# Kernel optimization log

Hardware: AMD Instinct MI355X
Metric: run time of the kernel (lower is better)

The kernel has to match this reference:

```python
import jax, jax.numpy as jnp
import numpy as np

K = 2  # DGL TAGConv default number of hops
N_GRAPHS = 64


def _tag_conv(h, src, dst, W, b, norm):
    # TAGConv: concat [h, A_hat h, A_hat^2 h] @ W + b, A_hat = D^-1/2 A D^-1/2
    n = h.shape[0]
    hops = [h]
    cur = h
    for _ in range(K):
        msg = (cur * norm)[src]                      # gather from src, [E, d]
        agg = jnp.zeros_like(cur).at[dst].add(msg)   # scatter-sum to dst
        cur = agg * norm
        hops.append(cur)
    z = jnp.concatenate(hops, axis=-1)               # [N, (K+1)*d]
    return jax.nn.relu(z @ W + b)


def _norm(dst, n):
    deg = jnp.zeros((n,), jnp.float32).at[dst].add(1.0)
    deg = jnp.clip(deg, 1.0, None)
    return (deg ** -0.5)[:, None]                    # [N, 1]


def setup_inputs() -> dict:
    key = jax.random.key(0)
    ks = jax.random.split(key, 8)
    N, E, IN, HID, C = 100000, 3200000, 128, 256, 10
    h = jax.random.normal(ks[0], (N, IN), jnp.float32)
    src = jax.random.randint(ks[1], (E,), 0, N, jnp.int32)
    dst = jax.random.randint(ks[2], (E,), 0, N, jnp.int32)
    graph_ids = jnp.sort(jax.random.randint(ks[3], (N,), 0, N_GRAPHS, jnp.int32))
    s1 = ((K + 1) * IN) ** -0.5
    s2 = ((K + 1) * HID) ** -0.5
    W1 = jax.random.normal(ks[4], ((K + 1) * IN, HID), jnp.float32) * s1
    b1 = jnp.zeros((HID,), jnp.float32)
    W2 = jax.random.normal(ks[5], ((K + 1) * HID, HID), jnp.float32) * s2
    b2 = jnp.zeros((HID,), jnp.float32)
    Wc = jax.random.normal(ks[6], (HID, C), jnp.float32) * (HID ** -0.5)
    bc = jnp.zeros((C,), jnp.float32)
    return {"h": h, "src": src, "dst": dst, "graph_ids": graph_ids,
            "W1": W1, "b1": b1, "W2": W2, "b2": b2, "Wc": Wc, "bc": bc}


def reference(h, src, dst, graph_ids, W1, b1, W2, b2, Wc, bc):
    n = h.shape[0]
    norm = _norm(dst, n)
    x = _tag_conv(h, src, dst, W1, b1, norm)
    x = _tag_conv(x, src, dst, W2, b2, norm)
    pooled = jax.ops.segment_max(x, graph_ids, num_segments=N_GRAPHS)  # [G, HID]
    return pooled @ Wc + bc                                            # [G, C]
```

## Files before the change

### kernel.cpp

```cpp
#include <hip/hip_runtime.h>
#include <hip/hip_bf16.h>


typedef unsigned short u16;
typedef unsigned int u32;
typedef unsigned char u8;

__device__ inline float u2f(u16 u) { return __uint_as_float(((u32)u) << 16); }
__device__ inline u16 f2u(float f) {
    __hip_bfloat16 b = __float2bfloat16(f);
    return *reinterpret_cast<u16*>(&b);
}


constexpr int NPB = 128, NC = 128, NBMAX = 784;

__global__ __launch_bounds__(256) void countA_kernel(
    const int* __restrict__ dst, int* __restrict__ Hmat, int E, int CS, int NB) {
    __shared__ int hist[NBMAX];
    int tid = threadIdx.x;
    for (int b = tid; b < NB; b += 256) hist[b] = 0;
    __syncthreads();
    int base = blockIdx.x * CS;
    int end = base + CS < E ? base + CS : E;
    for (int i = base + tid; i < end; i += 256) {
        int d = __builtin_nontemporal_load(dst + i);
        atomicAdd(&hist[d >> 7], 1);
    }
    __syncthreads();
    for (int b = tid; b < NB; b += 256) Hmat[b * NC + blockIdx.x] = hist[b];
}

__global__ __launch_bounds__(256) void scatterC_kernel(
    const int* __restrict__ src, const int* __restrict__ dst,
    const int* __restrict__ Omat, uint2* __restrict__ Earr,
    int E, int CS, int NB) {
    __shared__ int cur[NBMAX];
    int tid = threadIdx.x;
    int c = blockIdx.x;
    for (int b = tid; b < NB; b += 256) cur[b] = Omat[b * NC + c];
    __syncthreads();
    int base = c * CS;
    int end = base + CS < E ? base + CS : E;
    for (int i = base + tid; i < end; i += 256) {
        int d = __builtin_nontemporal_load(dst + i);
        int s = __builtin_nontemporal_load(src + i);
        int pos = atomicAdd(&cur[d >> 7], 1);
        uint2 e;
        e.x = (u32)s;
        e.y = (u32)(d & (NPB - 1));
        Earr[pos] = e;
    }
}

__global__ __launch_bounds__(256) void fineD_kernel(
    const uint2* __restrict__ Earr, const int* __restrict__ Omat,
    int* __restrict__ colidx, int* __restrict__ rowptr,
    float* __restrict__ normv, int N, int E, int NB) {
    __shared__ int cnt[NPB];
    __shared__ int scn[NPB];
    __shared__ int cur2[NPB];
    int tid = threadIdx.x;
    int b = blockIdx.x;
    int base = Omat[b * NC];
    int end = Omat[(b + 1) * NC];
    if (tid < NPB) cnt[tid] = 0;
    __syncthreads();
    for (int i = base + tid; i < end; i += 256)
        atomicAdd(&cnt[Earr[i].y], 1);
    __syncthreads();
    if (tid < NPB) scn[tid] = cnt[tid];
    __syncthreads();
    for (int off = 1; off < NPB; off <<= 1) {
        int v = (tid < NPB && tid >= off) ? scn[tid - off] : 0;
        __syncthreads();
        if (tid < NPB) scn[tid] += v;
        __syncthreads();
    }
    int node0 = b * NPB;
    if (tid < NPB) {
        int excl = scn[tid] - cnt[tid];
        cur2[tid] = base + excl;
        int node = node0 + tid;
        if (node < N) {
            rowptr[node] = base + excl;
            int d = cnt[tid];
            float fd = d < 1 ? 1.0f : (float)d;
            normv[node] = rsqrtf(fd);
        }
    }
    if (b == 0 && tid == 0) rowptr[N] = E;
    __syncthreads();
    for (int i = base + tid; i < end; i += 256) {
        uint2 e = Earr[i];
        int pos = atomicAdd(&cur2[e.y], 1);
        colidx[pos] = (int)e.x;
    }
}

__global__ void scan1_kernel(const int* __restrict__ in, int* __restrict__ outp,
                             int* __restrict__ bsum, int n) {
    __shared__ int sd[1024];
    int t = threadIdx.x;
    int i = blockIdx.x * 1024 + t;
    int v = (i < n) ? in[i] : 0;
    sd[t] = v;
    __syncthreads();
    for (int off = 1; off < 1024; off <<= 1) {
        int x = (t >= off) ? sd[t - off] : 0;
        __syncthreads();
        sd[t] += x;
        __syncthreads();
    }
    if (i < n) outp[i] = sd[t] - v;
    if (t == 1023) bsum[blockIdx.x] = sd[t];
}

__global__ void scan2_kernel(int* __restrict__ bsum, int nb) {
    __shared__ int sd[1024];
    int t = threadIdx.x;
    int v = (t < nb) ? bsum[t] : 0;
    sd[t] = v;
    __syncthreads();
    for (int off = 1; off < 1024; off <<= 1) {
        int x = (t >= off) ? sd[t - off] : 0;
        __syncthreads();
        sd[t] += x;
        __syncthreads();
    }
    if (t < nb) bsum[t] = sd[t] - v;
}

__global__ void scan3_kernel(int* __restrict__ outp, const int* __restrict__ bsum,
                             int n, int E) {
    int i = blockIdx.x * blockDim.x + threadIdx.x;
    if (i < n) outp[i] += bsum[i >> 10];
    if (i == 0) outp[n] = E;
}


struct alignas(4) U2 { u16 v[2]; };
struct alignas(8) U4 { u16 v[4]; };
struct alignas(16) U8 { u16 v[8]; };


__global__ __launch_bounds__(256) void castquant_f32_128(
    const float* __restrict__ h, u16* __restrict__ cat, int ldcat,
    const float* __restrict__ normv,
    u8* __restrict__ q, float* __restrict__ m, int N) {
    int row = blockIdx.x * 4 + (threadIdx.x >> 6);
    if (row >= N) return;
    int lane = threadIdx.x & 63;
    float2 f = *(const float2*)(h + (size_t)row * 128 + lane * 2);
    U2 o;
    o.v[0] = f2u(f.x);
    o.v[1] = f2u(f.y);
    *(U2*)(cat + (size_t)row * ldcat + lane * 2) = o;
    float mx = fmaxf(fabsf(f.x), fabsf(f.y));
    #pragma unroll
    for (int off = 32; off > 0; off >>= 1)
        mx = fmaxf(mx, __shfl_xor(mx, off, 64));
    float inv = mx > 0.f ? 127.f / mx : 0.f;
    u32 q0 = (u32)((int)rintf(f.x * inv) + 128);
    u32 q1 = (u32)((int)rintf(f.y * inv) + 128);
    *(unsigned short*)(q + (size_t)row * 128 + lane * 2) =
        (unsigned short)(q0 | (q1 << 8));
    if (lane == 0) m[row] = normv[row] * (mx * (1.f / 127.f));
}


__global__ __launch_bounds__(256) void quant_bf16_256(
    const u16* __restrict__ x, const float* __restrict__ normv,
    u8* __restrict__ q, float* __restrict__ m, int N) {
    int row = blockIdx.x * 4 + (threadIdx.x >> 6);
    if (row >= N) return;
    int lane = threadIdx.x & 63;
    U4 v = *(const U4*)(x + (size_t)row * 256 + lane * 4);
    float f[4];
    #pragma unroll
    for (int i = 0; i < 4; ++i) f[i] = u2f(v.v[i]);
    float mx = fmaxf(fmaxf(fabsf(f[0]), fabsf(f[1])),
                     fmaxf(fabsf(f[2]), fabsf(f[3])));
    #pragma unroll
    for (int off = 32; off > 0; off >>= 1)
        mx = fmaxf(mx, __shfl_xor(mx, off, 64));
    float inv = mx > 0.f ? 127.f / mx : 0.f;
    u32 b0 = (u32)((int)rintf(f[0] * inv) + 128);
    u32 b1 = (u32)((int)rintf(f[1] * inv) + 128);
    u32 b2 = (u32)((int)rintf(f[2] * inv) + 128);
    u32 b3 = (u32)((int)rintf(f[3] * inv) + 128);
    *(u32*)(q + (size_t)row * 256 + lane * 4) =
        b0 | (b1 << 8) | (b2 << 16) | (b3 << 24);
    if (lane == 0) m[row] = normv[row] * (mx * (1.f / 127.f));
}


template <int BPL, int QOUT>
__global__ __launch_bounds__(256, 2) void prop_q8_kernel(
    const u8* __restrict__ qin, const float* __restrict__ m,
    u16* __restrict__ out, int ldout,
    const int* __restrict__ rowptr, const int* __restrict__ colidx,
    const float* __restrict__ normv, int N,
    u8* __restrict__ qout, float* __restrict__ mout) {
    constexpr int D = 32 * BPL;
    constexpr int NW = BPL / 4;
    constexpr int UE = 8;
    int node = blockIdx.x * 4 + (threadIdx.x >> 6);
    if (node >= N) return;
    const int lane = threadIdx.x & 63;
    const int half = lane >> 5;
    const int l32 = lane & 31;
    const u32 laneoff = (u32)l32 * BPL;
    int s = rowptr[node], e = rowptr[node + 1];
    float acc[BPL];
    #pragma unroll
    for (int q = 0; q < BPL; ++q) acc[q] = 0.f;
    float msum = 0.f;
    const int nfull = (e - s) >> 4;
    int p = s;
    if (nfull > 0) {
        int c[UE];
        #pragma unroll
        for (int u = 0; u < UE; ++u) c[u] = colidx[s + 2 * u + half];
        for (int g = 0; g < nfull; ++g) {
            u32 w[UE][NW];
            #pragma unroll
            for (int u = 0; u < UE; ++u) {
                u32 off = (u32)c[u] * D + laneoff;
                if (BPL == 8) {
                    uint2 gg = *(const uint2*)(qin + off);
                    w[u][0] = gg.x; w[u][1] = gg.y;
                } else {
                    w[u][0] = *(const u32*)(qin + off);
                }
            }
            float nm[UE];
            #pragma unroll
            for (int u = 0; u < UE; ++u) nm[u] = m[c[u]];
            if (g + 1 < nfull) {
                int pn = s + (g + 1) * 16;
                #pragma unroll
                for (int u = 0; u < UE; ++u) c[u] = colidx[pn + 2 * u + half];
            }
            #pragma unroll
            for (int u = 0; u < UE; ++u) {
                msum += nm[u];
                #pragma unroll
                for (int t = 0; t < NW; ++t) {
                    u32 ww = w[u][t];
                    acc[4 * t + 0] += nm[u] * (float)(ww & 0xffu);
                    acc[4 * t + 1] += nm[u] * (float)((ww >> 8) & 0xffu);
                    acc[4 * t + 2] += nm[u] * (float)((ww >> 16) & 0xffu);
                    acc[4 * t + 3] += nm[u] * (float)(ww >> 24);
                }
            }
        }
        p = s + nfull * 16;
    }
    if (p < e) {
        const int el = e - 1;
        int c[UE];
        #pragma unroll
        for (int u = 0; u < UE; ++u) {
            int idx = p + 2 * u + half;
            c[u] = colidx[idx < e ? idx : el];
        }
        u32 w[UE][NW];
        #pragma unroll
        for (int u = 0; u < UE; ++u) {
            u32 off = (u32)c[u] * D + laneoff;
            if (BPL == 8) {
                uint2 gg = *(const uint2*)(qin + off);
                w[u][0] = gg.x; w[u][1] = gg.y;
            } else {
                w[u][0] = *(const u32*)(qin + off);
            }
        }
        float nm[UE];
        #pragma unroll
        for (int u = 0; u < UE; ++u) {
            int idx = p + 2 * u + half;
            float mm = m[c[u]];
            nm[u] = idx < e ? mm : 0.f;
        }
        #pragma unroll
        for (int u = 0; u < UE; ++u) {
            msum += nm[u];
            #pragma unroll
            for (int t = 0; t < NW; ++t) {
                u32 ww = w[u][t];
                acc[4 * t + 0] += nm[u] * (float)(ww & 0xffu);
                acc[4 * t + 1] += nm[u] * (float)((ww >> 8) & 0xffu);
                acc[4 * t + 2] += nm[u] * (float)((ww >> 16) & 0xffu);
                acc[4 * t + 3] += nm[u] * (float)(ww >> 24);
            }
        }
    }
    #pragma unroll
    for (int q = 0; q < BPL; ++q) acc[q] += __shfl_xor(acc[q], 32, 64);
    msum += __shfl_xor(msum, 32, 64);
    float nn = normv[node];
    #pragma unroll
    for (int q = 0; q < BPL; ++q) acc[q] = nn * (acc[q] - 128.f * msum);
    if (half == 0) {
        if (BPL == 8) {
            U8 o;
            #pragma unroll
            for (int q = 0; q < 8; ++q) o.v[q] = f2u(acc[q]);
            *(U8*)(out + (size_t)node * ldout + l32 * 8) = o;
        } else {
            U4 o;
            #pragma unroll
            for (int q = 0; q < 4; ++q) o.v[q] = f2u(acc[q]);
            *(U4*)(out + (size_t)node * ldout + l32 * 4) = o;
        }
    }
    if (QOUT) {
        float mx = 0.f;
        #pragma unroll
        for (int q = 0; q < BPL; ++q) mx = fmaxf(mx, fabsf(acc[q]));
        #pragma unroll
        for (int off = 16; off > 0; off >>= 1)
            mx = fmaxf(mx, __shfl_xor(mx, off, 64));
        float inv = mx > 0.f ? 127.f / mx : 0.f;
        if (half == 0) {
            u32 b[BPL > 4 ? 8 : 4];
            #pragma unroll
            for (int q = 0; q < BPL; ++q)
                b[q] = (u32)((int)rintf(acc[q] * inv) + 128);
            if (BPL == 8) {
                uint2 g;
                g.x = b[0] | (b[1] << 8) | (b[2] << 16) | (b[3] << 24);
                g.y = b[4] | (b[5] << 8) | (b[6] << 16) | (b[7] << 24);
                *(uint2*)(qout + (size_t)node * D + l32 * 8) = g;
            } else {
                *(u32*)(qout + (size_t)node * D + l32 * 4) =
                    b[0] | (b[1] << 8) | (b[2] << 16) | (b[3] << 24);
            }
            if (lane == 0) mout[node] = nn * (mx * (1.f / 127.f));
        }
    }
}


typedef __attribute__((ext_vector_type(8))) short bf16x8f;
typedef __attribute__((ext_vector_type(4))) float f32x4;

__device__ inline void async16(const void* g, void* l) {
    __builtin_amdgcn_global_load_lds(
        (__attribute__((address_space(1))) void*)(g),
        (__attribute__((address_space(3))) void*)(l), 16, 0, 0);
}

constexpr int GBM = 128, GBN = 128, GBK = 32, KH = 128;

template <int KK>
__global__ __launch_bounds__(256, 2) void gemm_mfma(
    const u16* __restrict__ A, int lda,
    const u16* __restrict__ Bt,
    const u16* __restrict__ Cadd,
    const float* __restrict__ bias,
    u16* __restrict__ Cout,
    int M, int relu) {
    constexpr int NPH = KK / KH;
    __shared__ u16 Ab[GBM * KH];
    __shared__ u16 Bb[GBN * KH];
    const int tid = threadIdx.x;
    const int lane = tid & 63;
    const int wave = tid >> 6;
    const int wm = wave >> 1, wn = wave & 1;
    int nwg = gridDim.x;
    int qq = nwg >> 3, rr = nwg & 7;
    int xcd = blockIdx.x & 7, wi = blockIdx.x >> 3;
    int nb = (xcd < rr ? xcd * (qq + 1) : rr * (qq + 1) + (xcd - rr) * qq) + wi;
    const int row0 = (nb >> 1) * GBM;
    const int col0 = (nb & 1) * GBN;
    const int NOUT = 256;

    f32x4 acc[4][4];
    #pragma unroll
    for (int mi = 0; mi < 4; ++mi)
        #pragma unroll
        for (int ni = 0; ni < 4; ++ni) acc[mi][ni] = (f32x4)0.f;

    const int mb = lane & 15;
    const int seg4 = lane >> 4;

    for (int ph = 0; ph < NPH; ++ph) {
        if (ph) __syncthreads();
        #pragma unroll
        for (int i = 0; i < 8; ++i) {
            int c = tid + i * 256;
            int row = c >> 4;
            int sg = (c & 15) ^ (row & 7);
            async16(A + (size_t)(row0 + row) * lda + ph * KH + sg * 8,
                    Ab + c * 8);
        }
        #pragma unroll
        for (int i = 0; i < 8; ++i) {
            int c = tid + i * 256;
            int row = c >> 4;
            int sg = (c & 15) ^ (row & 7);
            async16(Bt + (size_t)(col0 + row) * KK + ph * KH + sg * 8,
                    Bb + c * 8);
        }
        __syncthreads();
        #pragma unroll
        for (int ks = 0; ks < KH / GBK; ++ks) {
            int j = ks * 4 + seg4;
            bf16x8f a[4], b[4];
            #pragma unroll
            for (int mi = 0; mi < 4; ++mi) {
                int r = wm * 64 + mi * 16 + mb;
                int ca = r * 16 + (j ^ (r & 7));
                a[mi] = *(const bf16x8f*)&Ab[ca * 8];
            }
            #pragma unroll
            for (int ni = 0; ni < 4; ++ni) {
                int n = wn * 64 + ni * 16 + mb;
                int cb = n * 16 + (j ^ (n & 7));
                b[ni] = *(const bf16x8f*)&Bb[cb * 8];
            }
            #pragma unroll
            for (int mi = 0; mi < 4; ++mi)
                #pragma unroll
                for (int ni = 0; ni < 4; ++ni)
                    acc[mi][ni] = __builtin_amdgcn_mfma_f32_16x16x32_bf16(
                        a[mi], b[ni], acc[mi][ni], 0, 0, 0);
        }
    }

    #pragma unroll
    for (int mi = 0; mi < 4; ++mi) {
        #pragma unroll
        for (int r = 0; r < 4; ++r) {
            int row = row0 + wm * 64 + mi * 16 + (lane >> 4) * 4 + r;
            if (row < M) {
                #pragma unroll
                for (int ni = 0; ni < 4; ++ni) {
                    int col = col0 + wn * 64 + ni * 16 + (lane & 15);
                    float v = acc[mi][ni][r];
                    if (Cadd) v += u2f(Cadd[(size_t)row * NOUT + col]);
                    if (bias) v += bias[col];
                    if (relu) v = fmaxf(v, 0.f);
                    Cout[(size_t)row * NOUT + col] = f2u(v);
                }
            }
        }
    }
}

__global__ void transpose_cast(const float* __restrict__ W, u16* __restrict__ Wt,
                               int K, int Nn) {
    int idx = blockIdx.x * blockDim.x + threadIdx.x;
    if (idx < K * Nn) {
        int n = idx / K, k = idx % K;
        Wt[idx] = f2u(W[(size_t)k * Nn + n]);
    }
}


__global__ void pool_kernel(const u16* __restrict__ x, const int* __restrict__ gid,
                            float* __restrict__ pooled, int N, int HID) {
    int t = threadIdx.x;
    int n0 = blockIdx.x * 128;
    int n1 = n0 + 128 < N ? n0 + 128 : N;
    float cur = 0.f;
    int cg = gid[n0];
    for (int n = n0; n < n1; ++n) {
        int g = gid[n];
        if (g != cg) {
            atomicMax((int*)&pooled[(size_t)cg * HID + t], __float_as_int(cur));
            cg = g;
            cur = 0.f;
        }
        float v = u2f(x[(size_t)n * HID + t]);
        cur = cur > v ? cur : v;
    }
    atomicMax((int*)&pooled[(size_t)cg * HID + t], __float_as_int(cur));
}

__global__ void head_kernel(const float* __restrict__ pooled, const float* __restrict__ Wc,
                            const float* __restrict__ bc, float* __restrict__ out,
                            int HID, int C) {
    __shared__ float row[256];
    int g = blockIdx.x;
    int t = threadIdx.x;
    if (t < HID) row[t] = pooled[(size_t)g * HID + t];
    __syncthreads();
    if (t < C) {
        float s = bc[t];
        for (int k = 0; k < HID; ++k) s += row[k] * Wc[(size_t)k * C + t];
        out[(size_t)g * C + t] = s;
    }
}


extern "C" void kernel_launch(void* const* d_in, const int* in_sizes, int n_in,
                              void* d_out, int out_size, void* d_ws, size_t ws_size,
                              hipStream_t stream) {
    const float* h  = (const float*)d_in[0];
    const int* src  = (const int*)d_in[1];
    const int* dst  = (const int*)d_in[2];
    const int* gid  = (const int*)d_in[3];
    const float* W1 = (const float*)d_in[4];
    const float* b1 = (const float*)d_in[5];
    const float* W2 = (const float*)d_in[6];
    const float* b2 = (const float*)d_in[7];
    const float* Wc = (const float*)d_in[8];
    const float* bc = (const float*)d_in[9];
    float* out = (float*)d_out;

    const int N   = in_sizes[3];
    const int E   = in_sizes[1];
    const int IN  = in_sizes[0] / N;
    const int HID = in_sizes[5];
    const int C   = in_sizes[9];
    const int G   = out_size / C;
    const int CAT = 3 * IN;
    const int Mpad = (N + 127) & ~127;
    const int NB = (N + NPB - 1) / NPB;
    const int CS = (E + NC - 1) / NC;

    char* wp = (char*)d_ws;
    auto alloc = [&](size_t bytes) {
        char* p = wp;
        wp += (bytes + 255) & ~(size_t)255;
        return p;
    };
    float* pooled = (float*)alloc((size_t)G * HID * sizeof(float));
    float* normv  = (float*)alloc((size_t)N * sizeof(float));
    float* mv     = (float*)alloc((size_t)N * sizeof(float));
    float* mv2    = (float*)alloc((size_t)N * sizeof(float));
    int* rowptr   = (int*)alloc((size_t)(N + 1) * sizeof(int));
    int* bsum     = (int*)alloc(1024 * sizeof(int));
    int* Omat     = (int*)alloc((size_t)(NB * NC + 1) * sizeof(int));
    int* Hmat     = (int*)alloc((size_t)(NB * NC) * sizeof(int));
    int* colidx   = (int*)alloc((size_t)E * sizeof(int));
    u16* Wt1      = (u16*)alloc((size_t)CAT * HID * sizeof(u16));
    u16* Wt2      = (u16*)alloc((size_t)3 * HID * HID * sizeof(u16));
    u16* CAT1     = (u16*)alloc((size_t)Mpad * CAT * sizeof(u16));
    u16* X1       = (u16*)alloc((size_t)Mpad * HID * sizeof(u16));
    u16* B2       = (u16*)alloc((size_t)Mpad * HID * sizeof(u16));
    u16* B1       = CAT1;
    uint2* Earr   = (uint2*)CAT1;
    u8* Q8L2      = (u8*)(CAT1 + (size_t)Mpad * HID);
    u8* Q8A       = (u8*)B2;
    u8* Q8B       = (u8*)B2 + (size_t)Mpad * 128;

    const int n2 = NB * NC;
    countA_kernel<<<NC, 256, 0, stream>>>(dst, Hmat, E, CS, NB);
    scan1_kernel<<<(n2 + 1023) / 1024, 1024, 0, stream>>>(Hmat, Omat, bsum, n2);
    scan2_kernel<<<1, 1024, 0, stream>>>(bsum, (n2 + 1023) / 1024);
    scan3_kernel<<<(n2 + 255) / 256, 256, 0, stream>>>(Omat, bsum, n2, E);
    scatterC_kernel<<<NC, 256, 0, stream>>>(src, dst, Omat, Earr, E, CS, NB);
    fineD_kernel<<<NB, 256, 0, stream>>>(Earr, Omat, colidx, rowptr, normv, N, E, NB);

    transpose_cast<<<(CAT * HID + 255) / 256, 256, 0, stream>>>(W1, Wt1, CAT, HID);
    for (int s2 = 0; s2 < 3; ++s2)
        transpose_cast<<<(HID * HID + 255) / 256, 256, 0, stream>>>(
            W2 + (size_t)s2 * HID * HID, Wt2 + (size_t)s2 * HID * HID, HID, HID);

    int pb = (N + 3) / 4;
    castquant_f32_128<<<pb, 256, 0, stream>>>(h, CAT1, CAT, normv, Q8A, mv, N);
    prop_q8_kernel<4, 1><<<pb, 256, 0, stream>>>(Q8A, mv, CAT1 + IN, CAT,
                                                 rowptr, colidx, normv, N, Q8B, mv2);
    prop_q8_kernel<4, 0><<<pb, 256, 0, stream>>>(Q8B, mv2, CAT1 + 2 * IN, CAT,
                                                 rowptr, colidx, normv, N,
                                                 nullptr, nullptr);
    int nwg = (Mpad / GBM) * (HID / GBN);
    gemm_mfma<384><<<nwg, 256, 0, stream>>>(CAT1, CAT, Wt1, nullptr, b1, X1, N, 1);

    gemm_mfma<256><<<nwg, 256, 0, stream>>>(X1, HID, Wt2 + (size_t)2 * HID * HID,
                                            nullptr, nullptr, B1, N, 0);
    quant_bf16_256<<<pb, 256, 0, stream>>>(B1, normv, Q8L2, mv, N);
    prop_q8_kernel<8, 0><<<pb, 256, 0, stream>>>(Q8L2, mv, B2, HID,
                                                 rowptr, colidx, normv, N,
                                                 nullptr, nullptr);
    gemm_mfma<256><<<nwg, 256, 0, stream>>>(X1, HID, Wt2 + (size_t)HID * HID,
                                            B2, nullptr, B1, N, 0);
    quant_bf16_256<<<pb, 256, 0, stream>>>(B1, normv, Q8L2, mv, N);
    prop_q8_kernel<8, 0><<<pb, 256, 0, stream>>>(Q8L2, mv, B2, HID,
                                                 rowptr, colidx, normv, N,
                                                 nullptr, nullptr);
    gemm_mfma<256><<<nwg, 256, 0, stream>>>(X1, HID, Wt2, B2, b2, B1, N, 1);

    hipMemsetAsync(pooled, 0, (size_t)G * HID * sizeof(float), stream);
    pool_kernel<<<(N + 127) / 128, HID, 0, stream>>>(B1, gid, pooled, N, HID);
    head_kernel<<<G, HID, 0, stream>>>(pooled, Wc, bc, out, HID, C);
}
```

Baseline: 1.012 ms.

## Make GEMMs persistent with resident B tile and triple-buffered A pipeline

Replaces the one-tile-per-workgroup MFMA GEMM with a persistent kernel of 256 workgroups. Each workgroup loads its full 128-column weight slice into LDS once, then walks row tiles while streaming A through a three-stage async LDS ring with partial vmcnt waits. This removes repeated weight reloads and exposes load/compute overlap. The trade-off is much larger LDS use (occupancy 1), and it relies on a hardcoded 256-block grid and XCD slot mapping.

```diff
diff --git a/kernel.cpp b/kernel.cpp
--- a/kernel.cpp
+++ b/kernel.cpp
@@ -352,98 +352,116 @@
         (__attribute__((address_space(3))) void*)(l), 16, 0, 0);
 }
 
-constexpr int GBM = 128, GBN = 128, GBK = 32, KH = 128;
+constexpr int KPH = 64;
 
 template <int KK>
-__global__ __launch_bounds__(256, 2) void gemm_mfma(
+__global__ __launch_bounds__(256, 1) void gemm_persist(
     const u16* __restrict__ A, int lda,
     const u16* __restrict__ Bt,
     const u16* __restrict__ Cadd,
     const float* __restrict__ bias,
     u16* __restrict__ Cout,
-    int M, int relu) {
-    constexpr int NPH = KK / KH;
-    __shared__ u16 Ab[GBM * KH];
-    __shared__ u16 Bb[GBN * KH];
+    int M, int NRT, int relu) {
+    constexpr int KC = KK / 8;
+    constexpr int NPHT = KK / KPH;
+    __shared__ u16 Bb[128 * KK];
+    __shared__ u16 Ab[3][128 * KPH];
     const int tid = threadIdx.x;
     const int lane = tid & 63;
     const int wave = tid >> 6;
     const int wm = wave >> 1, wn = wave & 1;
-    int nwg = gridDim.x;
-    int qq = nwg >> 3, rr = nwg & 7;
-    int xcd = blockIdx.x & 7, wi = blockIdx.x >> 3;
-    int nb = (xcd < rr ? xcd * (qq + 1) : rr * (qq + 1) + (xcd - rr) * qq) + wi;
-    const int row0 = (nb >> 1) * GBM;
-    const int col0 = (nb & 1) * GBN;
+    const int slot = (blockIdx.x & 7) * 32 + (blockIdx.x >> 3);
+    const int r0 = slot >> 1;
+    const int col0 = (slot & 1) * 128;
     const int NOUT = 256;
 
-    f32x4 acc[4][4];
     #pragma unroll
-    for (int mi = 0; mi < 4; ++mi)
-        #pragma unroll
-        for (int ni = 0; ni < 4; ++ni) acc[mi][ni] = (f32x4)0.f;
+    for (int i = 0; i < 128 * KC / 256; ++i) {
+        int cb = tid + i * 256;
+        int n = cb / KC;
+        int sg = (cb % KC) ^ (n & 7);
+        async16(Bt + (size_t)(col0 + n) * KK + sg * 8, Bb + cb * 8);
+    }
+
+    const int nrt = (NRT - r0 + 127) >> 7;
+    const int ptot = nrt * NPHT;
+    auto stageA = [&](int p, int buf) {
+        int t = p / NPHT;
+        int ph = p - t * NPHT;
+        int rowb = (r0 + (t << 7)) << 7;
+        const u16* src = A + (size_t)rowb * lda + ph * KPH;
+        #pragma unroll
+        for (int i = 0; i < 4; ++i) {
+            int c = tid + i * 256;
+            int row = c >> 3;
+            int sg = (c & 7) ^ (row & 7);
+            async16(src + (size_t)row * lda + sg * 8, Ab[buf] + c * 8);
+        }
+    };
+    stageA(0, 0);
+    if (ptot > 1) stageA(1, 1);
 
     const int mb = lane & 15;
     const int seg4 = lane >> 4;
-
-    for (int ph = 0; ph < NPH; ++ph) {
-        if (ph) __syncthreads();
-        #pragma unroll
-        for (int i = 0; i < 8; ++i) {
-            int c = tid + i * 256;
-            int row = c >> 4;
-            int sg = (c & 15) ^ (row & 7);
-            async16(A + (size_t)(row0 + row) * lda + ph * KH + sg * 8,
-                    Ab + c * 8);
-        }
-        #pragma unroll
-        for (int i = 0; i < 8; ++i) {
-            int c = tid + i * 256;
-            int row = c >> 4;
-            int sg = (c & 15) ^ (row & 7);
-            async16(Bt + (size_t)(col0 + row) * KK + ph * KH + sg * 8,
-                    Bb + c * 8);
-        }
-        __syncthreads();
-        #pragma unroll
-        for (int ks = 0; ks < KH / GBK; ++ks) {
-            int j = ks * 4 + seg4;
-            bf16x8f a[4], b[4];
-            #pragma unroll
-            for (int mi = 0; mi < 4; ++mi) {
-                int r = wm * 64 + mi * 16 + mb;
-                int ca = r * 16 + (j ^ (r & 7));
-                a[mi] = *(const bf16x8f*)&Ab[ca * 8];
-            }
-            #pragma unroll
-            for (int ni = 0; ni < 4; ++ni) {
-                int n = wn * 64 + ni * 16 + mb;
-                int cb = n * 16 + (j ^ (n & 7));
-                b[ni] = *(const bf16x8f*)&Bb[cb * 8];
-            }
-            #pragma unroll
-            for (int mi = 0; mi < 4; ++mi)
+    int p = 0;
+    for (int t = 0; t < nrt; ++t) {
+        f32x4 acc[4][4];
+        #pragma unroll
+        for (int mi = 0; mi < 4; ++mi)
+            #pragma unroll
+            for (int ni = 0; ni < 4; ++ni) acc[mi][ni] = (f32x4)0.f;
+
+        #pragma unroll
+        for (int ph = 0; ph < NPHT; ++ph, ++p) {
+            if (p + 1 < ptot)
+                asm volatile("s_waitcnt vmcnt(4)" ::: "memory");
+            else
+                asm volatile("s_waitcnt vmcnt(0)" ::: "memory");
+            __builtin_amdgcn_s_barrier();
+            if (p + 2 < ptot) stageA(p + 2, (p + 2) % 3);
+            __builtin_amdgcn_sched_barrier(0);
+            const u16* Abuf = Ab[p % 3];
+            #pragma unroll
+            for (int ks = 0; ks < KPH / 32; ++ks) {
+                int jl = ks * 4 + seg4;
+                int jj = ph * (KPH / 8) + jl;
+                bf16x8f a[4], b[4];
                 #pragma unroll
-                for (int ni = 0; ni < 4; ++ni)
-                    acc[mi][ni] = __builtin_amdgcn_mfma_f32_16x16x32_bf16(
-                        a[mi], b[ni], acc[mi][ni], 0, 0, 0);
-        }
-    }
-
-    #pragma unroll
-    for (int mi = 0; mi < 4; ++mi) {
-        #pragma unroll
-        for (int r = 0; r < 4; ++r) {
-            int row = row0 + wm * 64 + mi * 16 + (lane >> 4) * 4 + r;
-            if (row < M) {
+                for (int mi = 0; mi < 4; ++mi) {
+                    int r = wm * 64 + mi * 16 + mb;
+                    int ca = r * 8 + (jl ^ (r & 7));
+                    a[mi] = *(const bf16x8f*)&Abuf[ca * 8];
+                }
                 #pragma unroll
                 for (int ni = 0; ni < 4; ++ni) {
-                    int col = col0 + wn * 64 + ni * 16 + (lane & 15);
-                    float v = acc[mi][ni][r];
-                    if (Cadd) v += u2f(Cadd[(size_t)row * NOUT + col]);
-                    if (bias) v += bias[col];
-                    if (relu) v = fmaxf(v, 0.f);
-                    Cout[(size_t)row * NOUT + col] = f2u(v);
+                    int n = wn * 64 + ni * 16 + mb;
+                    int cb = n * KC + (jj ^ (n & 7));
+                    b[ni] = *(const bf16x8f*)&Bb[cb * 8];
+                }
+                #pragma unroll
+                for (int mi = 0; mi < 4; ++mi)
+                    #pragma unroll
+                    for (int ni = 0; ni < 4; ++ni)
+                        acc[mi][ni] = __builtin_amdgcn_mfma_f32_16x16x32_bf16(
+                            a[mi], b[ni], acc[mi][ni], 0, 0, 0);
+            }
+        }
+        int rowb = (r0 + (t << 7)) << 7;
+        #pragma unroll
+        for (int mi = 0; mi < 4; ++mi) {
+            #pragma unroll
+            for (int r = 0; r < 4; ++r) {
+                int row = rowb + wm * 64 + mi * 16 + (lane >> 4) * 4 + r;
+                if (row < M) {
+                    #pragma unroll
+                    for (int ni = 0; ni < 4; ++ni) {
+                        int col = col0 + wn * 64 + ni * 16 + (lane & 15);
+                        float v = acc[mi][ni][r];
+                        if (Cadd) v += u2f(Cadd[(size_t)row * NOUT + col]);
+                        if (bias) v += bias[col];
+                        if (relu) v = fmaxf(v, 0.f);
+                        Cout[(size_t)row * NOUT + col] = f2u(v);
+                    }
                 }
             }
         }
@@ -568,22 +586,23 @@
     prop_q8_kernel<4, 0><<<pb, 256, 0, stream>>>(Q8B, mv2, CAT1 + 2 * IN, CAT,
                                                  rowptr, colidx, normv, N,
                                                  nullptr, nullptr);
-    int nwg = (Mpad / GBM) * (HID / GBN);
-    gemm_mfma<384><<<nwg, 256, 0, stream>>>(CAT1, CAT, Wt1, nullptr, b1, X1, N, 1);
-
-    gemm_mfma<256><<<nwg, 256, 0, stream>>>(X1, HID, Wt2 + (size_t)2 * HID * HID,
-                                            nullptr, nullptr, B1, N, 0);
+    const int NRT = Mpad / 128;
+    gemm_persist<384><<<256, 256, 0, stream>>>(CAT1, CAT, Wt1, nullptr, b1,
+                                               X1, N, NRT, 1);
+
+    gemm_persist<256><<<256, 256, 0, stream>>>(X1, HID, Wt2 + (size_t)2 * HID * HID,
+                                               nullptr, nullptr, B1, N, NRT, 0);
     quant_bf16_256<<<pb, 256, 0, stream>>>(B1, normv, Q8L2, mv, N);
     prop_q8_kernel<8, 0><<<pb, 256, 0, stream>>>(Q8L2, mv, B2, HID,
                                                  rowptr, colidx, normv, N,
                                                  nullptr, nullptr);
-    gemm_mfma<256><<<nwg, 256, 0, stream>>>(X1, HID, Wt2 + (size_t)HID * HID,
-                                            B2, nullptr, B1, N, 0);
+    gemm_persist<256><<<256, 256, 0, stream>>>(X1, HID, Wt2 + (size_t)HID * HID,
+                                               B2, nullptr, B1, N, NRT, 0);
     quant_bf16_256<<<pb, 256, 0, stream>>>(B1, normv, Q8L2, mv, N);
     prop_q8_kernel<8, 0><<<pb, 256, 0, stream>>>(Q8L2, mv, B2, HID,
                                                  rowptr, colidx, normv, N,
                                                  nullptr, nullptr);
-    gemm_mfma<256><<<nwg, 256, 0, stream>>>(X1, HID, Wt2, B2, b2, B1, N, 1);
+    gemm_persist<256><<<256, 256, 0, stream>>>(X1, HID, Wt2, B2, b2, B1, N, NRT, 1);
 
     hipMemsetAsync(pooled, 0, (size_t)G * HID * sizeof(float), stream);
     pool_kernel<<<(N + 127) / 128, HID, 0, stream>>>(B1, gid, pooled, N, HID);
```

Result: slower. 1.157 ms (+14.3%).
